# Kernel optimization log

Hardware: AMD Instinct MI355X
Metric: run time of the kernel (lower is better)

The kernel has to match this reference:

```python
import jax, jax.numpy as jnp
import numpy as np

NUM_ROUNDS = 3


def squash(x, axis=-1):
    # s_norm / (1 + s_norm) * x / sqrt(s_norm), matching the torch code exactly
    s_norm = jnp.sum(x * x, axis=axis, keepdims=True)
    return (s_norm / (1.0 + s_norm)) * x / jnp.sqrt(s_norm)


def setup_inputs() -> dict:
    key = jax.random.key(0)
    k1, k2 = jax.random.split(key)
    x = jax.random.normal(k1, (512, 1152, 8), dtype=jnp.float32)   # [B, R, Cin]
    W = jax.random.normal(k2, (10, 1152, 8, 16), dtype=jnp.float32)  # [N, R, Cin, Cout]
    return {"x": x, "W": W}


def reference(x, W):
    # priors = x[None,:,:,None,:] @ W[:,None,:,:,:]  -> [N, B, R, 1, Cout]
    priors = jnp.einsum('bri,nrio->nbro', x, W)[:, :, :, None, :]
    logits = jnp.zeros_like(priors)  # [N, B, R, 1, Cout]
    outps = None
    for i in range(NUM_ROUNDS):
        probs = jax.nn.softmax(logits, axis=2)  # softmax over routes R
        outps = squash(jnp.sum(probs * priors, axis=2, keepdims=True))  # [N, B, 1, 1, Cout]
        if i != NUM_ROUNDS - 1:
            # agreement logit update: dot over Cout
            logits = logits + jnp.sum(priors * outps, axis=-1, keepdims=True)
    return outps
```

## Files before the change

### kernel.cpp

```cpp
#include <hip/hip_runtime.h>
#include <math.h>

#define R_ROUTES 1152
#define CIN 8
#define COUT 16
#define BATCH 512
#define NCAPS 10
#define NUM_ROUNDS 3

#define WP_U32S (NCAPS * R_ROUTES * COUT * 4)
#define XP_U32S (BATCH * R_ROUTES * 4)
#define WS_NEED ((size_t)(WP_U32S + XP_U32S) * 4)

typedef __fp16 h2 __attribute__((ext_vector_type(2)));
union U32H2 { unsigned int u; h2 h; };

__device__ __forceinline__ unsigned int pkrtz(float lo, float hi) {
    U32H2 v; v.h = __builtin_amdgcn_cvt_pkrtz(lo, hi);
    return v.u;
}
__device__ __forceinline__ h2 as_h2(unsigned int u) { U32H2 v; v.u = u; return v.h; }
__device__ __forceinline__ float f_lo(unsigned int u) { return (float)as_h2(u).x; }
__device__ __forceinline__ float f_hi(unsigned int u) { return (float)as_h2(u).y; }
__device__ __forceinline__ float dot2(unsigned int p, unsigned int s, float c) {
    return __builtin_amdgcn_fdot2(as_h2(p), as_h2(s), c, false);
}

__device__ __forceinline__ int sunit(int r, int h) {
    return (2 * r + h) ^ ((r >> 2) & 7);
}

extern "C" __global__ void __launch_bounds__(256)
pack_wx(const float* __restrict__ W, const float* __restrict__ x,
        unsigned int* __restrict__ Wp, unsigned int* __restrict__ xp)
{
    const int bid = blockIdx.x;
    if (bid < NCAPS * R_ROUTES * COUT / 256) {
        const int tau = bid * 256 + threadIdx.x;
        const int o = tau & 15;
        const int nr = tau >> 4;
        const float* __restrict__ src = W + (size_t)nr * 128 + o;
        uint4 u;
        u.x = pkrtz(src[0],  src[16]);
        u.y = pkrtz(src[32], src[48]);
        u.z = pkrtz(src[64], src[80]);
        u.w = pkrtz(src[96], src[112]);
        *(uint4*)(Wp + (size_t)tau * 4) = u;
    } else {
        const int idx = (bid - NCAPS * R_ROUTES * COUT / 256) * 256 + threadIdx.x;
        const float4 v0 = *(const float4*)(x + (size_t)idx * 8);
        const float4 v1 = *(const float4*)(x + (size_t)idx * 8 + 4);
        uint4 u;
        u.x = pkrtz(v0.x, v0.y); u.y = pkrtz(v0.z, v0.w);
        u.z = pkrtz(v1.x, v1.y); u.w = pkrtz(v1.z, v1.w);
        *(uint4*)(xp + (size_t)idx * 4) = u;
    }
}

extern "C" __global__ void __launch_bounds__(512, 4)
capsule_routing_v13(const unsigned int* __restrict__ xp,
                    const unsigned int* __restrict__ Wp,
                    float* __restrict__ out)
{
    __shared__ unsigned int pbuf[2 * R_ROUTES * 8];
    __shared__ float wred[16 * 16];
    __shared__ float red[2 * 32 * 20];
    __shared__ float sred[2 * 4];
    __shared__ float sv[2 * 16];

    const int blk = blockIdx.x;
    const int n = blk >> 8;
    const int bp = blk & 255;
    const int t = threadIdx.x;

    const unsigned int* __restrict__ xp0 = xp + (size_t)(2 * bp) * (R_ROUTES * 4);
    const unsigned int* __restrict__ xp1 = xp0 + R_ROUTES * 4;
    const unsigned int* __restrict__ Wn = Wp + (size_t)n * (R_ROUTES * 64);

    float cs00 = 0.f, cs01 = 0.f, cs02 = 0.f, cs03 = 0.f;
    float cs10 = 0.f, cs11 = 0.f, cs12 = 0.f, cs13 = 0.f;
    {
        const int q = t >> 2;
        const int oq = t & 3;
        const int subw = (oq & 1) * 2;
        const int hq = oq >> 1;

        #pragma unroll 1
        for (int it = 0; it < 9; ++it) {
            const int r = it * 128 + q;
            const unsigned int* __restrict__ wb = Wn + (size_t)r * 64 + oq * 4;
            const uint4 w0 = *(const uint4*)(wb);
            const uint4 w1 = *(const uint4*)(wb + 16);
            const uint4 w2 = *(const uint4*)(wb + 32);
            const uint4 w3 = *(const uint4*)(wb + 48);
            const uint4 xa = *(const uint4*)(xp0 + (size_t)r * 4);
            const uint4 xb = *(const uint4*)(xp1 + (size_t)r * 4);

            {
                const float p0 = dot2(w0.w, xa.w, dot2(w0.z, xa.z, dot2(w0.y, xa.y, dot2(w0.x, xa.x, 0.f))));
                const float p1 = dot2(w1.w, xa.w, dot2(w1.z, xa.z, dot2(w1.y, xa.y, dot2(w1.x, xa.x, 0.f))));
                const float p2 = dot2(w2.w, xa.w, dot2(w2.z, xa.z, dot2(w2.y, xa.y, dot2(w2.x, xa.x, 0.f))));
                const float p3 = dot2(w3.w, xa.w, dot2(w3.z, xa.z, dot2(w3.y, xa.y, dot2(w3.x, xa.x, 0.f))));
                cs00 += p0; cs01 += p1; cs02 += p2; cs03 += p3;
                uint2 u; u.x = pkrtz(p0, p1); u.y = pkrtz(p2, p3);
                *(uint2*)(pbuf + sunit(r, hq) * 4 + subw) = u;
            }
            {
                const float p0 = dot2(w0.w, xb.w, dot2(w0.z, xb.z, dot2(w0.y, xb.y, dot2(w0.x, xb.x, 0.f))));
                const float p1 = dot2(w1.w, xb.w, dot2(w1.z, xb.z, dot2(w1.y, xb.y, dot2(w1.x, xb.x, 0.f))));
                const float p2 = dot2(w2.w, xb.w, dot2(w2.z, xb.z, dot2(w2.y, xb.y, dot2(w2.x, xb.x, 0.f))));
                const float p3 = dot2(w3.w, xb.w, dot2(w3.z, xb.z, dot2(w3.y, xb.y, dot2(w3.x, xb.x, 0.f))));
                cs10 += p0; cs11 += p1; cs12 += p2; cs13 += p3;
                uint2 u; u.x = pkrtz(p0, p1); u.y = pkrtz(p2, p3);
                *(uint2*)(pbuf + R_ROUTES * 8 + sunit(r, hq) * 4 + subw) = u;
            }
        }

        #pragma unroll
        for (int mask = 4; mask <= 32; mask <<= 1) {
            cs00 += __shfl_xor(cs00, mask, 64); cs01 += __shfl_xor(cs01, mask, 64);
            cs02 += __shfl_xor(cs02, mask, 64); cs03 += __shfl_xor(cs03, mask, 64);
            cs10 += __shfl_xor(cs10, mask, 64); cs11 += __shfl_xor(cs11, mask, 64);
            cs12 += __shfl_xor(cs12, mask, 64); cs13 += __shfl_xor(cs13, mask, 64);
        }
        if ((t & 63) < 4) {
            const int w = t >> 6;
            *(float4*)(wred + (w * 2 + 0) * 16 + 4 * oq) = make_float4(cs00, cs01, cs02, cs03);
            *(float4*)(wred + (w * 2 + 1) * 16 + 4 * oq) = make_float4(cs10, cs11, cs12, cs13);
        }
    }
    __syncthreads();

    const int half = t >> 8;
    const int tt = t & 255;
    unsigned int* __restrict__ pb = pbuf + half * (R_ROUTES * 8);
    float* __restrict__ redh = red + half * (32 * 20);
    float* __restrict__ sredh = sred + half * 4;
    float* __restrict__ svh = sv + half * 16;

    if (tt < 16) {
        float s = 0.f;
        #pragma unroll
        for (int w = 0; w < 8; ++w) s += wred[(w * 2 + half) * 16 + tt];
        svh[tt] = s * (1.0f / (float)R_ROUTES);
    }
    __syncthreads();

    float sn = 0.f;
    #pragma unroll
    for (int o = 0; o < 16; ++o) { const float s = svh[o]; sn = fmaf(s, s, sn); }
    float factor = sn / ((1.0f + sn) * sqrtf(sn));

    const int nr = (tt < 128) ? 5 : 4;
    float bl[5] = {0.f, 0.f, 0.f, 0.f, 0.f};

    #pragma unroll 1
    for (int pass = 1; pass < NUM_ROUNDS; ++pass) {
        unsigned int svp[8];
        #pragma unroll
        for (int s = 0; s < 8; ++s)
            svp[s] = pkrtz(svh[2 * s], svh[2 * s + 1]);
        float acc[16];
        #pragma unroll
        for (int o = 0; o < 16; ++o) acc[o] = 0.f;
        float es = 0.f;

        #pragma unroll
        for (int k = 0; k < 5; ++k) {
            if (k < nr) {
                const int r = tt + (k << 8);
                const uint4 a = *(const uint4*)(pb + sunit(r, 0) * 4);
                const uint4 c = *(const uint4*)(pb + sunit(r, 1) * 4);
                float d = 0.f;
                d = dot2(a.x, svp[0], d);
                d = dot2(a.y, svp[1], d);
                d = dot2(a.z, svp[2], d);
                d = dot2(a.w, svp[3], d);
                d = dot2(c.x, svp[4], d);
                d = dot2(c.y, svp[5], d);
                d = dot2(c.z, svp[6], d);
                d = dot2(c.w, svp[7], d);
                bl[k] = fmaf(factor, d, bl[k]);
                const float e = __expf(bl[k]);
                es += e;
                acc[0]  = fmaf(e, f_lo(a.x), acc[0]);
                acc[1]  = fmaf(e, f_hi(a.x), acc[1]);
                acc[2]  = fmaf(e, f_lo(a.y), acc[2]);
                acc[3]  = fmaf(e, f_hi(a.y), acc[3]);
                acc[4]  = fmaf(e, f_lo(a.z), acc[4]);
                acc[5]  = fmaf(e, f_hi(a.z), acc[5]);
                acc[6]  = fmaf(e, f_lo(a.w), acc[6]);
                acc[7]  = fmaf(e, f_hi(a.w), acc[7]);
                acc[8]  = fmaf(e, f_lo(c.x), acc[8]);
                acc[9]  = fmaf(e, f_hi(c.x), acc[9]);
                acc[10] = fmaf(e, f_lo(c.y), acc[10]);
                acc[11] = fmaf(e, f_hi(c.y), acc[11]);
                acc[12] = fmaf(e, f_lo(c.z), acc[12]);
                acc[13] = fmaf(e, f_hi(c.z), acc[13]);
                acc[14] = fmaf(e, f_lo(c.w), acc[14]);
                acc[15] = fmaf(e, f_hi(c.w), acc[15]);
            }
        }
        #pragma unroll
        for (int off = 32; off > 0; off >>= 1) es += __shfl_xor(es, off, 64);
        if ((t & 63) == 0) sredh[tt >> 6] = es;

        #pragma unroll
        for (int o = 0; o < 16; ++o) {
            acc[o] += __shfl_xor(acc[o], 1, 64);
            acc[o] += __shfl_xor(acc[o], 2, 64);
            acc[o] += __shfl_xor(acc[o], 4, 64);
        }
        if ((tt & 7) == 0) {
            float* dst = redh + (tt >> 3) * 20;
            *(float4*)(dst + 0)  = make_float4(acc[0],  acc[1],  acc[2],  acc[3]);
            *(float4*)(dst + 4)  = make_float4(acc[4],  acc[5],  acc[6],  acc[7]);
            *(float4*)(dst + 8)  = make_float4(acc[8],  acc[9],  acc[10], acc[11]);
            *(float4*)(dst + 12) = make_float4(acc[12], acc[13], acc[14], acc[15]);
        }
        __syncthreads();

        if (pass < NUM_ROUNDS - 1) {
            if (tt < 16) {
                float s = 0.f;
                #pragma unroll
                for (int w = 0; w < 32; ++w) s += redh[w * 20 + tt];
                const float Z = sredh[0] + sredh[1] + sredh[2] + sredh[3];
                svh[tt] = s / Z;
            }
            __syncthreads();

            sn = 0.f;
            #pragma unroll
            for (int o = 0; o < 16; ++o) { const float s = svh[o]; sn = fmaf(s, s, sn); }
            factor = sn / ((1.0f + sn) * sqrtf(sn));
        } else {
            if (tt < 16) {
                float s = 0.f;
                #pragma unroll
                for (int w = 0; w < 32; ++w) s += redh[w * 20 + tt];
                const float Z = sredh[0] + sredh[1] + sredh[2] + sredh[3];
                const float sv_o = s / Z;
                float sq = sv_o * sv_o;
                sq += __shfl_xor(sq, 1, 64);
                sq += __shfl_xor(sq, 2, 64);
                sq += __shfl_xor(sq, 4, 64);
                sq += __shfl_xor(sq, 8, 64);
                const float f2 = sq / ((1.0f + sq) * sqrtf(sq));
                const int o = (tt >> 2) + ((tt & 3) << 2);
                out[((size_t)n * BATCH + 2 * bp + half) * COUT + o] = f2 * sv_o;
            }
        }
    }
}

extern "C" __global__ void __launch_bounds__(256)
pack_w_only(const float* __restrict__ W, unsigned int* __restrict__ Wp)
{
    const int tau = blockIdx.x * 256 + threadIdx.x;
    const int o = tau & 15;
    const int nr = tau >> 4;
    const float* __restrict__ src = W + (size_t)nr * 128 + o;
    uint4 u;
    u.x = pkrtz(src[0],  src[16]);
    u.y = pkrtz(src[32], src[48]);
    u.z = pkrtz(src[64], src[80]);
    u.w = pkrtz(src[96], src[112]);
    *(uint4*)(Wp + (size_t)tau * 4) = u;
}

extern "C" __global__ void __launch_bounds__(512, 4)
capsule_routing_v9f(const float* __restrict__ x,
                    const unsigned int* __restrict__ Wp,
                    float* __restrict__ out)
{
    __shared__ unsigned int pbuf[2 * R_ROUTES * 8];
    __shared__ float wred[16 * 16];
    __shared__ float red[2 * 32 * 20];
    __shared__ float sred[2 * 4];
    __shared__ float sv[2 * 16];

    const int blk = blockIdx.x;
    const int n = blk >> 8;
    const int bp = blk & 255;
    const int t = threadIdx.x;

    const float* __restrict__ x0 = x + (size_t)(2 * bp) * (R_ROUTES * CIN);
    const float* __restrict__ x1 = x0 + R_ROUTES * CIN;
    const unsigned int* __restrict__ Wn = Wp + (size_t)n * (R_ROUTES * 64);

    float cs00 = 0.f, cs01 = 0.f, cs02 = 0.f, cs03 = 0.f;
    float cs10 = 0.f, cs11 = 0.f, cs12 = 0.f, cs13 = 0.f;
    {
        const int q = t >> 2;
        const int oq = t & 3;
        const int subw = (oq & 1) * 2;
        const int hq = oq >> 1;

        #pragma unroll 1
        for (int it = 0; it < 9; ++it) {
            const int r = it * 128 + q;
            const unsigned int* __restrict__ wb = Wn + (size_t)r * 64 + oq * 4;
            const uint4 w0 = *(const uint4*)(wb);
            const uint4 w1 = *(const uint4*)(wb + 16);
            const uint4 w2 = *(const uint4*)(wb + 32);
            const uint4 w3 = *(const uint4*)(wb + 48);
            const float4 xa0 = *(const float4*)(x0 + r * 8);
            const float4 xa1 = *(const float4*)(x0 + r * 8 + 4);
            const float4 xb0 = *(const float4*)(x1 + r * 8);
            const float4 xb1 = *(const float4*)(x1 + r * 8 + 4);
            {
                const unsigned int xq0 = pkrtz(xa0.x, xa0.y), xq1 = pkrtz(xa0.z, xa0.w);
                const unsigned int xq2 = pkrtz(xa1.x, xa1.y), xq3 = pkrtz(xa1.z, xa1.w);
                const float p0 = dot2(w0.w, xq3, dot2(w0.z, xq2, dot2(w0.y, xq1, dot2(w0.x, xq0, 0.f))));
                const float p1 = dot2(w1.w, xq3, dot2(w1.z, xq2, dot2(w1.y, xq1, dot2(w1.x, xq0, 0.f))));
                const float p2 = dot2(w2.w, xq3, dot2(w2.z, xq2, dot2(w2.y, xq1, dot2(w2.x, xq0, 0.f))));
                const float p3 = dot2(w3.w, xq3, dot2(w3.z, xq2, dot2(w3.y, xq1, dot2(w3.x, xq0, 0.f))));
                cs00 += p0; cs01 += p1; cs02 += p2; cs03 += p3;
                uint2 u; u.x = pkrtz(p0, p1); u.y = pkrtz(p2, p3);
                *(uint2*)(pbuf + sunit(r, hq) * 4 + subw) = u;
            }
            {
                const unsigned int xq0 = pkrtz(xb0.x, xb0.y), xq1 = pkrtz(xb0.z, xb0.w);
                const unsigned int xq2 = pkrtz(xb1.x, xb1.y), xq3 = pkrtz(xb1.z, xb1.w);
                const float p0 = dot2(w0.w, xq3, dot2(w0.z, xq2, dot2(w0.y, xq1, dot2(w0.x, xq0, 0.f))));
                const float p1 = dot2(w1.w, xq3, dot2(w1.z, xq2, dot2(w1.y, xq1, dot2(w1.x, xq0, 0.f))));
                const float p2 = dot2(w2.w, xq3, dot2(w2.z, xq2, dot2(w2.y, xq1, dot2(w2.x, xq0, 0.f))));
                const float p3 = dot2(w3.w, xq3, dot2(w3.z, xq2, dot2(w3.y, xq1, dot2(w3.x, xq0, 0.f))));
                cs10 += p0; cs11 += p1; cs12 += p2; cs13 += p3;
                uint2 u; u.x = pkrtz(p0, p1); u.y = pkrtz(p2, p3);
                *(uint2*)(pbuf + R_ROUTES * 8 + sunit(r, hq) * 4 + subw) = u;
            }
        }
        #pragma unroll
        for (int mask = 4; mask <= 32; mask <<= 1) {
            cs00 += __shfl_xor(cs00, mask, 64); cs01 += __shfl_xor(cs01, mask, 64);
            cs02 += __shfl_xor(cs02, mask, 64); cs03 += __shfl_xor(cs03, mask, 64);
            cs10 += __shfl_xor(cs10, mask, 64); cs11 += __shfl_xor(cs11, mask, 64);
            cs12 += __shfl_xor(cs12, mask, 64); cs13 += __shfl_xor(cs13, mask, 64);
        }
        if ((t & 63) < 4) {
            const int w = t >> 6;
            *(float4*)(wred + (w * 2 + 0) * 16 + 4 * oq) = make_float4(cs00, cs01, cs02, cs03);
            *(float4*)(wred + (w * 2 + 1) * 16 + 4 * oq) = make_float4(cs10, cs11, cs12, cs13);
        }
    }
    __syncthreads();

    const int half = t >> 8;
    const int tt = t & 255;
    unsigned int* __restrict__ pb = pbuf + half * (R_ROUTES * 8);
    float* __restrict__ redh = red + half * (32 * 20);
    float* __restrict__ sredh = sred + half * 4;
    float* __restrict__ svh = sv + half * 16;

    if (tt < 16) {
        float s = 0.f;
        #pragma unroll
        for (int w = 0; w < 8; ++w) s += wred[(w * 2 + half) * 16 + tt];
        svh[tt] = s * (1.0f / (float)R_ROUTES);
    }
    __syncthreads();

    float sn = 0.f;
    #pragma unroll
    for (int o = 0; o < 16; ++o) { const float s = svh[o]; sn = fmaf(s, s, sn); }
    float factor = sn / ((1.0f + sn) * sqrtf(sn));

    const int nr = (tt < 128) ? 5 : 4;
    float bl[5] = {0.f, 0.f, 0.f, 0.f, 0.f};

    #pragma unroll 1
    for (int pass = 1; pass < NUM_ROUNDS; ++pass) {
        unsigned int svp[8];
        #pragma unroll
        for (int s = 0; s < 8; ++s) svp[s] = pkrtz(svh[2 * s], svh[2 * s + 1]);
        float acc[16];
        #pragma unroll
        for (int o = 0; o < 16; ++o) acc[o] = 0.f;
        float es = 0.f;
        #pragma unroll
        for (int k = 0; k < 5; ++k) {
            if (k < nr) {
                const int r = tt + (k << 8);
                const uint4 a = *(const uint4*)(pb + sunit(r, 0) * 4);
                const uint4 c = *(const uint4*)(pb + sunit(r, 1) * 4);
                float d = 0.f;
                d = dot2(a.x, svp[0], d); d = dot2(a.y, svp[1], d);
                d = dot2(a.z, svp[2], d); d = dot2(a.w, svp[3], d);
                d = dot2(c.x, svp[4], d); d = dot2(c.y, svp[5], d);
                d = dot2(c.z, svp[6], d); d = dot2(c.w, svp[7], d);
                bl[k] = fmaf(factor, d, bl[k]);
                const float e = __expf(bl[k]);
                es += e;
                acc[0]  = fmaf(e, f_lo(a.x), acc[0]);  acc[1]  = fmaf(e, f_hi(a.x), acc[1]);
                acc[2]  = fmaf(e, f_lo(a.y), acc[2]);  acc[3]  = fmaf(e, f_hi(a.y), acc[3]);
                acc[4]  = fmaf(e, f_lo(a.z), acc[4]);  acc[5]  = fmaf(e, f_hi(a.z), acc[5]);
                acc[6]  = fmaf(e, f_lo(a.w), acc[6]);  acc[7]  = fmaf(e, f_hi(a.w), acc[7]);
                acc[8]  = fmaf(e, f_lo(c.x), acc[8]);  acc[9]  = fmaf(e, f_hi(c.x), acc[9]);
                acc[10] = fmaf(e, f_lo(c.y), acc[10]); acc[11] = fmaf(e, f_hi(c.y), acc[11]);
                acc[12] = fmaf(e, f_lo(c.z), acc[12]); acc[13] = fmaf(e, f_hi(c.z), acc[13]);
                acc[14] = fmaf(e, f_lo(c.w), acc[14]); acc[15] = fmaf(e, f_hi(c.w), acc[15]);
            }
        }
        #pragma unroll
        for (int off = 32; off > 0; off >>= 1) es += __shfl_xor(es, off, 64);
        if ((t & 63) == 0) sredh[tt >> 6] = es;
        #pragma unroll
        for (int o = 0; o < 16; ++o) {
            acc[o] += __shfl_xor(acc[o], 1, 64);
            acc[o] += __shfl_xor(acc[o], 2, 64);
            acc[o] += __shfl_xor(acc[o], 4, 64);
        }
        if ((tt & 7) == 0) {
            float* dst = redh + (tt >> 3) * 20;
            *(float4*)(dst + 0)  = make_float4(acc[0],  acc[1],  acc[2],  acc[3]);
            *(float4*)(dst + 4)  = make_float4(acc[4],  acc[5],  acc[6],  acc[7]);
            *(float4*)(dst + 8)  = make_float4(acc[8],  acc[9],  acc[10], acc[11]);
            *(float4*)(dst + 12) = make_float4(acc[12], acc[13], acc[14], acc[15]);
        }
        __syncthreads();
        if (tt < 16) {
            float s = 0.f;
            #pragma unroll
            for (int w = 0; w < 32; ++w) s += redh[w * 20 + tt];
            const float Z = sredh[0] + sredh[1] + sredh[2] + sredh[3];
            svh[tt] = s / Z;
        }
        __syncthreads();
        sn = 0.f;
        #pragma unroll
        for (int o = 0; o < 16; ++o) { const float s = svh[o]; sn = fmaf(s, s, sn); }
        factor = sn / ((1.0f + sn) * sqrtf(sn));
    }

    if (tt < 16) {
        const int o = (tt >> 2) + ((tt & 3) << 2);
        out[((size_t)n * BATCH + 2 * bp + half) * COUT + o] = factor * svh[tt];
    }
}

extern "C" void kernel_launch(void* const* d_in, const int* in_sizes, int n_in,
                              void* d_out, int out_size, void* d_ws, size_t ws_size,
                              hipStream_t stream) {
    const float* x = (const float*)d_in[0];
    const float* W = (const float*)d_in[1];
    float* out = (float*)d_out;
    unsigned int* Wp = (unsigned int*)d_ws;
    unsigned int* xp = Wp + WP_U32S;

    if (ws_size >= WS_NEED) {
        const int wblocks = NCAPS * R_ROUTES * COUT / 256;
        const int xblocks = BATCH * R_ROUTES / 256;
        pack_wx<<<dim3(wblocks + xblocks), dim3(256), 0, stream>>>(W, x, Wp, xp);
        capsule_routing_v13<<<dim3(NCAPS * (BATCH / 2)), dim3(512), 0, stream>>>(xp, Wp, out);
    } else {
        pack_w_only<<<dim3(NCAPS * R_ROUTES * COUT / 256), dim3(256), 0, stream>>>(W, Wp);
        capsule_routing_v9f<<<dim3(NCAPS * (BATCH / 2)), dim3(512), 0, stream>>>(x, Wp, out);
    }
}
```

Before: 137.6 us.

## Process four batch rows per block to reuse each W load across more rows

Each block now handles four batch elements per capsule with 1024 threads instead of two with 512, so every fp16 W fragment loaded from global memory feeds four prior computations instead of two. The routing phase gives each batch element 256 threads, and the reduction widens by one shuffle step. This halves W traffic per output and halves the block count. In exchange the block needs more shared memory and registers, which may lower occupancy, and there are fewer blocks to spread across CUs.

```diff
diff --git a/kernel.cpp b/kernel.cpp
--- a/kernel.cpp
+++ b/kernel.cpp
@@ -11,6 +11,7 @@
 #define WP_U32S (NCAPS * R_ROUTES * COUT * 4)
 #define XP_U32S (BATCH * R_ROUTES * 4)
 #define WS_NEED ((size_t)(WP_U32S + XP_U32S) * 4)
+#define PB_B 9216
 
 typedef __fp16 h2 __attribute__((ext_vector_type(2)));
 union U32H2 { unsigned int u; h2 h; };
@@ -57,28 +58,42 @@
     }
 }
 
-extern "C" __global__ void __launch_bounds__(512, 4)
-capsule_routing_v13(const unsigned int* __restrict__ xp,
+#define DOROW(XV, CS0, CS1, CS2, CS3, PBASE)                               \
+    {                                                                      \
+        const float p0 = dot2(w0.w, XV.w, dot2(w0.z, XV.z, dot2(w0.y, XV.y, dot2(w0.x, XV.x, 0.f)))); \
+        const float p1 = dot2(w1.w, XV.w, dot2(w1.z, XV.z, dot2(w1.y, XV.y, dot2(w1.x, XV.x, 0.f)))); \
+        const float p2 = dot2(w2.w, XV.w, dot2(w2.z, XV.z, dot2(w2.y, XV.y, dot2(w2.x, XV.x, 0.f)))); \
+        const float p3 = dot2(w3.w, XV.w, dot2(w3.z, XV.z, dot2(w3.y, XV.y, dot2(w3.x, XV.x, 0.f)))); \
+        CS0 += p0; CS1 += p1; CS2 += p2; CS3 += p3;                        \
+        uint2 u_; u_.x = pkrtz(p0, p1); u_.y = pkrtz(p2, p3);              \
+        *(uint2*)((PBASE) + sunit(r, hq) * 4 + subw) = u_;                 \
+    }
+
+extern "C" __global__ void __launch_bounds__(1024, 4)
+capsule_routing_v14(const unsigned int* __restrict__ xp,
                     const unsigned int* __restrict__ Wp,
                     float* __restrict__ out)
 {
-    __shared__ unsigned int pbuf[2 * R_ROUTES * 8];
-    __shared__ float wred[16 * 16];
-    __shared__ float red[2 * 32 * 20];
-    __shared__ float sred[2 * 4];
-    __shared__ float sv[2 * 16];
+    __shared__ unsigned int pbuf[4 * PB_B];
+    __shared__ float redu[4 * 16 * 20];
+    __shared__ float sred[4 * 4];
+    __shared__ float sv[4 * 16];
 
     const int blk = blockIdx.x;
-    const int n = blk >> 8;
-    const int bp = blk & 255;
+    const int n = blk >> 7;
+    const int bq = blk & 127;
     const int t = threadIdx.x;
 
-    const unsigned int* __restrict__ xp0 = xp + (size_t)(2 * bp) * (R_ROUTES * 4);
-    const unsigned int* __restrict__ xp1 = xp0 + R_ROUTES * 4;
+    const unsigned int* __restrict__ xq0 = xp + (size_t)(4 * bq) * (R_ROUTES * 4);
+    const unsigned int* __restrict__ xq1 = xq0 + R_ROUTES * 4;
+    const unsigned int* __restrict__ xq2 = xq1 + R_ROUTES * 4;
+    const unsigned int* __restrict__ xq3 = xq2 + R_ROUTES * 4;
     const unsigned int* __restrict__ Wn = Wp + (size_t)n * (R_ROUTES * 64);
 
     float cs00 = 0.f, cs01 = 0.f, cs02 = 0.f, cs03 = 0.f;
     float cs10 = 0.f, cs11 = 0.f, cs12 = 0.f, cs13 = 0.f;
+    float cs20 = 0.f, cs21 = 0.f, cs22 = 0.f, cs23 = 0.f;
+    float cs30 = 0.f, cs31 = 0.f, cs32 = 0.f, cs33 = 0.f;
     {
         const int q = t >> 2;
         const int oq = t & 3;
@@ -86,34 +101,37 @@
         const int hq = oq >> 1;
 
         #pragma unroll 1
-        for (int it = 0; it < 9; ++it) {
-            const int r = it * 128 + q;
+        for (int it = 0; it < 4; ++it) {
+            const int r = it * 256 + q;
             const unsigned int* __restrict__ wb = Wn + (size_t)r * 64 + oq * 4;
             const uint4 w0 = *(const uint4*)(wb);
             const uint4 w1 = *(const uint4*)(wb + 16);
             const uint4 w2 = *(const uint4*)(wb + 32);
             const uint4 w3 = *(const uint4*)(wb + 48);
-            const uint4 xa = *(const uint4*)(xp0 + (size_t)r * 4);
-            const uint4 xb = *(const uint4*)(xp1 + (size_t)r * 4);
-
-            {
-                const float p0 = dot2(w0.w, xa.w, dot2(w0.z, xa.z, dot2(w0.y, xa.y, dot2(w0.x, xa.x, 0.f))));
-                const float p1 = dot2(w1.w, xa.w, dot2(w1.z, xa.z, dot2(w1.y, xa.y, dot2(w1.x, xa.x, 0.f))));
-                const float p2 = dot2(w2.w, xa.w, dot2(w2.z, xa.z, dot2(w2.y, xa.y, dot2(w2.x, xa.x, 0.f))));
-                const float p3 = dot2(w3.w, xa.w, dot2(w3.z, xa.z, dot2(w3.y, xa.y, dot2(w3.x, xa.x, 0.f))));
-                cs00 += p0; cs01 += p1; cs02 += p2; cs03 += p3;
-                uint2 u; u.x = pkrtz(p0, p1); u.y = pkrtz(p2, p3);
-                *(uint2*)(pbuf + sunit(r, hq) * 4 + subw) = u;
-            }
-            {
-                const float p0 = dot2(w0.w, xb.w, dot2(w0.z, xb.z, dot2(w0.y, xb.y, dot2(w0.x, xb.x, 0.f))));
-                const float p1 = dot2(w1.w, xb.w, dot2(w1.z, xb.z, dot2(w1.y, xb.y, dot2(w1.x, xb.x, 0.f))));
-                const float p2 = dot2(w2.w, xb.w, dot2(w2.z, xb.z, dot2(w2.y, xb.y, dot2(w2.x, xb.x, 0.f))));
-                const float p3 = dot2(w3.w, xb.w, dot2(w3.z, xb.z, dot2(w3.y, xb.y, dot2(w3.x, xb.x, 0.f))));
-                cs10 += p0; cs11 += p1; cs12 += p2; cs13 += p3;
-                uint2 u; u.x = pkrtz(p0, p1); u.y = pkrtz(p2, p3);
-                *(uint2*)(pbuf + R_ROUTES * 8 + sunit(r, hq) * 4 + subw) = u;
-            }
+            const uint4 xa = *(const uint4*)(xq0 + (size_t)r * 4);
+            const uint4 xb = *(const uint4*)(xq1 + (size_t)r * 4);
+            const uint4 xc = *(const uint4*)(xq2 + (size_t)r * 4);
+            const uint4 xd = *(const uint4*)(xq3 + (size_t)r * 4);
+            DOROW(xa, cs00, cs01, cs02, cs03, pbuf);
+            DOROW(xb, cs10, cs11, cs12, cs13, pbuf + PB_B);
+            DOROW(xc, cs20, cs21, cs22, cs23, pbuf + 2 * PB_B);
+            DOROW(xd, cs30, cs31, cs32, cs33, pbuf + 3 * PB_B);
+        }
+        if (t < 512) {
+            const int r = 1024 + q;
+            const unsigned int* __restrict__ wb = Wn + (size_t)r * 64 + oq * 4;
+            const uint4 w0 = *(const uint4*)(wb);
+            const uint4 w1 = *(const uint4*)(wb + 16);
+            const uint4 w2 = *(const uint4*)(wb + 32);
+            const uint4 w3 = *(const uint4*)(wb + 48);
+            const uint4 xa = *(const uint4*)(xq0 + (size_t)r * 4);
+            const uint4 xb = *(const uint4*)(xq1 + (size_t)r * 4);
+            const uint4 xc = *(const uint4*)(xq2 + (size_t)r * 4);
+            const uint4 xd = *(const uint4*)(xq3 + (size_t)r * 4);
+            DOROW(xa, cs00, cs01, cs02, cs03, pbuf);
+            DOROW(xb, cs10, cs11, cs12, cs13, pbuf + PB_B);
+            DOROW(xc, cs20, cs21, cs22, cs23, pbuf + 2 * PB_B);
+            DOROW(xd, cs30, cs31, cs32, cs33, pbuf + 3 * PB_B);
         }
 
         #pragma unroll
@@ -122,33 +140,39 @@
             cs02 += __shfl_xor(cs02, mask, 64); cs03 += __shfl_xor(cs03, mask, 64);
             cs10 += __shfl_xor(cs10, mask, 64); cs11 += __shfl_xor(cs11, mask, 64);
             cs12 += __shfl_xor(cs12, mask, 64); cs13 += __shfl_xor(cs13, mask, 64);
+            cs20 += __shfl_xor(cs20, mask, 64); cs21 += __shfl_xor(cs21, mask, 64);
+            cs22 += __shfl_xor(cs22, mask, 64); cs23 += __shfl_xor(cs23, mask, 64);
+            cs30 += __shfl_xor(cs30, mask, 64); cs31 += __shfl_xor(cs31, mask, 64);
+            cs32 += __shfl_xor(cs32, mask, 64); cs33 += __shfl_xor(cs33, mask, 64);
         }
         if ((t & 63) < 4) {
             const int w = t >> 6;
-            *(float4*)(wred + (w * 2 + 0) * 16 + 4 * oq) = make_float4(cs00, cs01, cs02, cs03);
-            *(float4*)(wred + (w * 2 + 1) * 16 + 4 * oq) = make_float4(cs10, cs11, cs12, cs13);
+            *(float4*)(redu + (w * 4 + 0) * 16 + 4 * oq) = make_float4(cs00, cs01, cs02, cs03);
+            *(float4*)(redu + (w * 4 + 1) * 16 + 4 * oq) = make_float4(cs10, cs11, cs12, cs13);
+            *(float4*)(redu + (w * 4 + 2) * 16 + 4 * oq) = make_float4(cs20, cs21, cs22, cs23);
+            *(float4*)(redu + (w * 4 + 3) * 16 + 4 * oq) = make_float4(cs30, cs31, cs32, cs33);
         }
     }
     __syncthreads();
 
-    const int half = t >> 8;
+    const int quarter = t >> 8;
     const int tt = t & 255;
-    unsigned int* __restrict__ pb = pbuf + half * (R_ROUTES * 8);
-    float* __restrict__ redh = red + half * (32 * 20);
-    float* __restrict__ sredh = sred + half * 4;
-    float* __restrict__ svh = sv + half * 16;
+    unsigned int* __restrict__ pb = pbuf + quarter * PB_B;
+    float* __restrict__ redq = redu + quarter * (16 * 20);
+    float* __restrict__ sredq = sred + quarter * 4;
+    float* __restrict__ svq = sv + quarter * 16;
 
     if (tt < 16) {
         float s = 0.f;
         #pragma unroll
-        for (int w = 0; w < 8; ++w) s += wred[(w * 2 + half) * 16 + tt];
-        svh[tt] = s * (1.0f / (float)R_ROUTES);
+        for (int w = 0; w < 16; ++w) s += redu[(w * 4 + quarter) * 16 + tt];
+        svq[tt] = s * (1.0f / (float)R_ROUTES);
     }
     __syncthreads();
 
     float sn = 0.f;
     #pragma unroll
-    for (int o = 0; o < 16; ++o) { const float s = svh[o]; sn = fmaf(s, s, sn); }
+    for (int o = 0; o < 16; ++o) { const float s = svq[o]; sn = fmaf(s, s, sn); }
     float factor = sn / ((1.0f + sn) * sqrtf(sn));
 
     const int nr = (tt < 128) ? 5 : 4;
@@ -159,7 +183,7 @@
         unsigned int svp[8];
         #pragma unroll
         for (int s = 0; s < 8; ++s)
-            svp[s] = pkrtz(svh[2 * s], svh[2 * s + 1]);
+            svp[s] = pkrtz(svq[2 * s], svq[2 * s + 1]);
         float acc[16];
         #pragma unroll
         for (int o = 0; o < 16; ++o) acc[o] = 0.f;
@@ -203,16 +227,17 @@
         }
         #pragma unroll
         for (int off = 32; off > 0; off >>= 1) es += __shfl_xor(es, off, 64);
-        if ((t & 63) == 0) sredh[tt >> 6] = es;
+        if ((t & 63) == 0) sredq[tt >> 6] = es;
 
         #pragma unroll
         for (int o = 0; o < 16; ++o) {
             acc[o] += __shfl_xor(acc[o], 1, 64);
             acc[o] += __shfl_xor(acc[o], 2, 64);
             acc[o] += __shfl_xor(acc[o], 4, 64);
-        }
-        if ((tt & 7) == 0) {
-            float* dst = redh + (tt >> 3) * 20;
+            acc[o] += __shfl_xor(acc[o], 8, 64);
+        }
+        if ((tt & 15) == 0) {
+            float* dst = redq + (tt >> 4) * 20;
             *(float4*)(dst + 0)  = make_float4(acc[0],  acc[1],  acc[2],  acc[3]);
             *(float4*)(dst + 4)  = make_float4(acc[4],  acc[5],  acc[6],  acc[7]);
             *(float4*)(dst + 8)  = make_float4(acc[8],  acc[9],  acc[10], acc[11]);
@@ -224,22 +249,22 @@
             if (tt < 16) {
                 float s = 0.f;
                 #pragma unroll
-                for (int w = 0; w < 32; ++w) s += redh[w * 20 + tt];
-                const float Z = sredh[0] + sredh[1] + sredh[2] + sredh[3];
-                svh[tt] = s / Z;
+                for (int w = 0; w < 16; ++w) s += redq[w * 20 + tt];
+                const float Z = sredq[0] + sredq[1] + sredq[2] + sredq[3];
+                svq[tt] = s / Z;
             }
             __syncthreads();
 
             sn = 0.f;
             #pragma unroll
-            for (int o = 0; o < 16; ++o) { const float s = svh[o]; sn = fmaf(s, s, sn); }
+            for (int o = 0; o < 16; ++o) { const float s = svq[o]; sn = fmaf(s, s, sn); }
             factor = sn / ((1.0f + sn) * sqrtf(sn));
         } else {
             if (tt < 16) {
                 float s = 0.f;
                 #pragma unroll
-                for (int w = 0; w < 32; ++w) s += redh[w * 20 + tt];
-                const float Z = sredh[0] + sredh[1] + sredh[2] + sredh[3];
+                for (int w = 0; w < 16; ++w) s += redq[w * 20 + tt];
+                const float Z = sredq[0] + sredq[1] + sredq[2] + sredq[3];
                 const float sv_o = s / Z;
                 float sq = sv_o * sv_o;
                 sq += __shfl_xor(sq, 1, 64);
@@ -248,7 +273,7 @@
                 sq += __shfl_xor(sq, 8, 64);
                 const float f2 = sq / ((1.0f + sq) * sqrtf(sq));
                 const int o = (tt >> 2) + ((tt & 3) << 2);
-                out[((size_t)n * BATCH + 2 * bp + half) * COUT + o] = f2 * sv_o;
+                out[((size_t)n * BATCH + 4 * bq + quarter) * COUT + o] = f2 * sv_o;
             }
         }
     }
@@ -277,8 +302,8 @@
     __shared__ unsigned int pbuf[2 * R_ROUTES * 8];
     __shared__ float wred[16 * 16];
     __shared__ float red[2 * 32 * 20];
-    __shared__ float sred[2 * 4];
-    __shared__ float sv[2 * 16];
+    __shared__ float sred2[2 * 4];
+    __shared__ float sv2[2 * 16];
 
     const int blk = blockIdx.x;
     const int n = blk >> 8;
@@ -310,23 +335,23 @@
             const float4 xb0 = *(const float4*)(x1 + r * 8);
             const float4 xb1 = *(const float4*)(x1 + r * 8 + 4);
             {
-                const unsigned int xq0 = pkrtz(xa0.x, xa0.y), xq1 = pkrtz(xa0.z, xa0.w);
-                const unsigned int xq2 = pkrtz(xa1.x, xa1.y), xq3 = pkrtz(xa1.z, xa1.w);
-                const float p0 = dot2(w0.w, xq3, dot2(w0.z, xq2, dot2(w0.y, xq1, dot2(w0.x, xq0, 0.f))));
-                const float p1 = dot2(w1.w, xq3, dot2(w1.z, xq2, dot2(w1.y, xq1, dot2(w1.x, xq0, 0.f))));
-                const float p2 = dot2(w2.w, xq3, dot2(w2.z, xq2, dot2(w2.y, xq1, dot2(w2.x, xq0, 0.f))));
-                const float p3 = dot2(w3.w, xq3, dot2(w3.z, xq2, dot2(w3.y, xq1, dot2(w3.x, xq0, 0.f))));
+                const unsigned int xv0 = pkrtz(xa0.x, xa0.y), xv1 = pkrtz(xa0.z, xa0.w);
+                const unsigned int xv2 = pkrtz(xa1.x, xa1.y), xv3 = pkrtz(xa1.z, xa1.w);
+                const float p0 = dot2(w0.w, xv3, dot2(w0.z, xv2, dot2(w0.y, xv1, dot2(w0.x, xv0, 0.f))));
+                const float p1 = dot2(w1.w, xv3, dot2(w1.z, xv2, dot2(w1.y, xv1, dot2(w1.x, xv0, 0.f))));
+                const float p2 = dot2(w2.w, xv3, dot2(w2.z, xv2, dot2(w2.y, xv1, dot2(w2.x, xv0, 0.f))));
+                const float p3 = dot2(w3.w, xv3, dot2(w3.z, xv2, dot2(w3.y, xv1, dot2(w3.x, xv0, 0.f))));
                 cs00 += p0; cs01 += p1; cs02 += p2; cs03 += p3;
                 uint2 u; u.x = pkrtz(p0, p1); u.y = pkrtz(p2, p3);
                 *(uint2*)(pbuf + sunit(r, hq) * 4 + subw) = u;
             }
             {
-                const unsigned int xq0 = pkrtz(xb0.x, xb0.y), xq1 = pkrtz(xb0.z, xb0.w);
-                const unsigned int xq2 = pkrtz(xb1.x, xb1.y), xq3 = pkrtz(xb1.z, xb1.w);
-                const float p0 = dot2(w0.w, xq3, dot2(w0.z, xq2, dot2(w0.y, xq1, dot2(w0.x, xq0, 0.f))));
-                const float p1 = dot2(w1.w, xq3, dot2(w1.z, xq2, dot2(w1.y, xq1, dot2(w1.x, xq0, 0.f))));
-                const float p2 = dot2(w2.w, xq3, dot2(w2.z, xq2, dot2(w2.y, xq1, dot2(w2.x, xq0, 0.f))));
-                const float p3 = dot2(w3.w, xq3, dot2(w3.z, xq2, dot2(w3.y, xq1, dot2(w3.x, xq0, 0.f))));
+                const unsigned int xv0 = pkrtz(xb0.x, xb0.y), xv1 = pkrtz(xb0.z, xb0.w);
+                const unsigned int xv2 = pkrtz(xb1.x, xb1.y), xv3 = pkrtz(xb1.z, xb1.w);
+                const float p0 = dot2(w0.w, xv3, dot2(w0.z, xv2, dot2(w0.y, xv1, dot2(w0.x, xv0, 0.f))));
+                const float p1 = dot2(w1.w, xv3, dot2(w1.z, xv2, dot2(w1.y, xv1, dot2(w1.x, xv0, 0.f))));
+                const float p2 = dot2(w2.w, xv3, dot2(w2.z, xv2, dot2(w2.y, xv1, dot2(w2.x, xv0, 0.f))));
+                const float p3 = dot2(w3.w, xv3, dot2(w3.z, xv2, dot2(w3.y, xv1, dot2(w3.x, xv0, 0.f))));
                 cs10 += p0; cs11 += p1; cs12 += p2; cs13 += p3;
                 uint2 u; u.x = pkrtz(p0, p1); u.y = pkrtz(p2, p3);
                 *(uint2*)(pbuf + R_ROUTES * 8 + sunit(r, hq) * 4 + subw) = u;
@@ -351,8 +376,8 @@
     const int tt = t & 255;
     unsigned int* __restrict__ pb = pbuf + half * (R_ROUTES * 8);
     float* __restrict__ redh = red + half * (32 * 20);
-    float* __restrict__ sredh = sred + half * 4;
-    float* __restrict__ svh = sv + half * 16;
+    float* __restrict__ sredh = sred2 + half * 4;
+    float* __restrict__ svh = sv2 + half * 16;
 
     if (tt < 16) {
         float s = 0.f;
@@ -453,7 +478,7 @@
         const int wblocks = NCAPS * R_ROUTES * COUT / 256;
         const int xblocks = BATCH * R_ROUTES / 256;
         pack_wx<<<dim3(wblocks + xblocks), dim3(256), 0, stream>>>(W, x, Wp, xp);
-        capsule_routing_v13<<<dim3(NCAPS * (BATCH / 2)), dim3(512), 0, stream>>>(xp, Wp, out);
+        capsule_routing_v14<<<dim3(NCAPS * (BATCH / 4)), dim3(1024), 0, stream>>>(xp, Wp, out);
     } else {
         pack_w_only<<<dim3(NCAPS * R_ROUTES * COUT / 256), dim3(256), 0, stream>>>(W, Wp);
         capsule_routing_v9f<<<dim3(NCAPS * (BATCH / 2)), dim3(512), 0, stream>>>(x, Wp, out);
```

Result: slower. 155.0 us (+12.6%).
